# Performance work log

Hardware: AMD Instinct MI355X
Metric: run time of the kernel (lower is better)

Reference implementation:

```python
import jax, jax.numpy as jnp
import numpy as np


def _igd(x, pf):
    # pf: [M, d] reference front, x: [N, d] candidate set
    # squared Euclidean distances via ||a||^2 + ||b||^2 - 2 a.b (cdist expansion)
    pf_sq = jnp.sum(pf * pf, axis=1, keepdims=True)          # [M, 1]
    x_sq = jnp.sum(x * x, axis=1, keepdims=True).T            # [1, N]
    cross = pf @ x.T                                          # [M, N]
    d2 = jnp.maximum(pf_sq + x_sq - 2.0 * cross, 0.0)
    dist = jnp.sqrt(d2)                                       # [M, N]
    # IGD: mean over reference points of min distance to candidate set
    return jnp.mean(jnp.min(dist, axis=1))


def setup_inputs() -> dict:
    key = jax.random.key(0)
    k1, k2 = jax.random.split(key)
    N, M, D = 16384, 16384, 64
    x = jax.random.normal(k1, (N, D), dtype=jnp.float32)
    pf = jax.random.normal(k2, (M, D), dtype=jnp.float32)
    return {"x": x, "pf": pf}


def reference(x, pf):
    return _igd(x, pf)
```

## Files before the change

kernel.cpp:

```cpp
#include <hip/hip_runtime.h>


typedef float f32x16 __attribute__((ext_vector_type(16)));
typedef float f32x2 __attribute__((ext_vector_type(2)));
typedef int i32x8 __attribute__((ext_vector_type(8)));
typedef unsigned long long u64;

#define DIM 64
#define NSPLIT 12
#define UNITB 2048
#define MTILE 256

union BFrag { u64 q[4]; i32x8 v; };

__device__ __forceinline__ void encode16(const float* f, u64 w[2], float& sumsq) {
    unsigned int w32[4];
#pragma unroll
    for (int k = 0; k < 4; ++k) {
        int lo = __builtin_amdgcn_cvt_pk_fp8_f32(f[4 * k],     f[4 * k + 1], 0,  false);
        w32[k] = __builtin_amdgcn_cvt_pk_fp8_f32(f[4 * k + 2], f[4 * k + 3], lo, true);
    }
#pragma unroll
    for (int k = 0; k < 4; ++k) {
        f32x2 d0 = __builtin_amdgcn_cvt_pk_f32_fp8(w32[k], false);
        f32x2 d1 = __builtin_amdgcn_cvt_pk_f32_fp8(w32[k], true);
        sumsq += d0.x * d0.x + d0.y * d0.y + d1.x * d1.x + d1.y * d1.y;
    }
    w[0] = (u64)w32[0] | ((u64)w32[1] << 32);
    w[1] = (u64)w32[2] | ((u64)w32[3] << 32);
}

__global__ void pack_kernel(const float* __restrict__ x, const float* __restrict__ pf,
                            unsigned char* __restrict__ Bp, unsigned char* __restrict__ Ab,
                            float* __restrict__ xsq, float* __restrict__ pfsq,
                            float* __restrict__ out, int N, int M) {
    int gid = blockIdx.x * blockDim.x + threadIdx.x;
    if (gid == 0) out[0] = 0.f;
    if (gid < N * 4) {
        int col = gid >> 2, t = gid & 3;
        const float* s = x + (size_t)col * DIM + t * 16;
        float4 v0 = *(const float4*)(s);
        float4 v1 = *(const float4*)(s + 4);
        float4 v2 = *(const float4*)(s + 8);
        float4 v3 = *(const float4*)(s + 12);
        float f[16] = {v0.x, v0.y, v0.z, v0.w, v1.x, v1.y, v1.z, v1.w,
                       v2.x, v2.y, v2.z, v2.w, v3.x, v3.y, v3.z, v3.w};
        float partial = 0.f;
        u64 w[2];
        encode16(f, w, partial);
        int u = col >> 5, c31 = col & 31;
        unsigned char* ub = Bp + (size_t)u * UNITB;
        int h = t >> 1;
#pragma unroll
        for (int ss = 0; ss < 2; ++ss) {
            int q = (t & 1) * 2 + ss;
            *(u64*)(ub + (size_t)q * 512 + (size_t)(h * 32 + c31) * 8) = w[ss];
        }
        partial += __shfl_xor(partial, 1);
        partial += __shfl_xor(partial, 2);
        if (t == 0) xsq[col] = partial;
    } else {
        int g = gid - N * 4;
        int row = g >> 2, q = g & 3;
        if (row >= M) return;
        const float* s = pf + (size_t)row * DIM + q * 16;
        float4 v0 = *(const float4*)(s);
        float4 v1 = *(const float4*)(s + 4);
        float4 v2 = *(const float4*)(s + 8);
        float4 v3 = *(const float4*)(s + 12);
        float f[16] = {v0.x, v0.y, v0.z, v0.w, v1.x, v1.y, v1.z, v1.w,
                       v2.x, v2.y, v2.z, v2.w, v3.x, v3.y, v3.z, v3.w};
#pragma unroll
        for (int j = 0; j < 16; ++j) f[j] *= -2.f;
        float partial = 0.f;
        u64 w[2];
        encode16(f, w, partial);
        *(u64*)(Ab + (size_t)row * DIM + q * 16)     = w[0];
        *(u64*)(Ab + (size_t)row * DIM + q * 16 + 8) = w[1];
        partial += __shfl_xor(partial, 1);
        partial += __shfl_xor(partial, 2);
        if (q == 0) pfsq[row] = partial * 0.25f;
    }
}

__global__ __launch_bounds__(256, 3)
void igd_main(const unsigned char* __restrict__ A, const unsigned char* __restrict__ Bp,
              const float* __restrict__ xsq, float* __restrict__ partial, int N) {
    const int tid = threadIdx.x;
    const int mTile  = blockIdx.x;
    const int nsplit = blockIdx.y;
    const int lane = tid & 63;
    const int wave = tid >> 6;
    const int half = lane >> 5;
    const int l31  = lane & 31;
    const int rowBase = mTile * MTILE + wave * 64;

    const int utotal = N / 32;
    const int ubase  = utotal / NSPLIT;
    const int urem   = utotal % NSPLIT;
    const int ustart = nsplit * ubase + (nsplit < urem ? nsplit : urem);
    const int ucount = ubase + (nsplit < urem ? 1 : 0);

    BFrag a[2];
#pragma unroll
    for (int g = 0; g < 2; ++g) {
        const unsigned char* ap = A + (size_t)(rowBase + 32 * g + l31) * DIM + half * 32;
#pragma unroll
        for (int qq = 0; qq < 4; ++qq)
            a[g].q[qq] = *(const u64*)(ap + qq * 8);
    }

    const unsigned char* bG = Bp + (size_t)ustart * UNITB + lane * 8;
    const float* xG = xsq + ustart * 32 + l31;

#define LOADG(rr, u)                                                           \
    {                                                                          \
        const unsigned char* p = bG + (size_t)(u) * UNITB;                     \
        rr.q[0] = *(const u64*)(p);                                            \
        rr.q[1] = *(const u64*)(p + 512);                                      \
        rr.q[2] = *(const u64*)(p + 1024);                                     \
        rr.q[3] = *(const u64*)(p + 1536);                                     \
    }

    f32x16 zero, m0, m1;
#pragma unroll
    for (int r = 0; r < 16; ++r) { zero[r] = 0.f; m0[r] = 1e30f; m1[r] = 1e30f; }

#define MFMA2(accA, accB, bfrag)                                               \
    {                                                                          \
        accA = __builtin_amdgcn_mfma_scale_f32_32x32x64_f8f6f4(                \
            a[0].v, bfrag.v, zero, 0, 0, 0, 0x7F7F7F7F, 0, 0x7F7F7F7F);        \
        accB = __builtin_amdgcn_mfma_scale_f32_32x32x64_f8f6f4(                \
            a[1].v, bfrag.v, zero, 0, 0, 0, 0x7F7F7F7F, 0, 0x7F7F7F7F);        \
    }

#define MINS(accA, accB, xq0)                                                  \
    {                                                                          \
        _Pragma("unroll")                                                      \
        for (int r = 0; r < 16; ++r) {                                         \
            m0[r] = fminf(m0[r], accA[r] + (xq0));                             \
            m1[r] = fminf(m1[r], accB[r] + (xq0));                             \
        }                                                                      \
    }

    BFrag b[4];
    float xq[4];
#pragma unroll
    for (int i = 0; i < 4; ++i) {
        LOADG(b[i], i);
        xq[i] = xG[(size_t)i * 32];
    }

    const int umain = ucount & ~3;
    for (int u = 0; u < umain; u += 4) {
#pragma unroll
        for (int s = 0; s < 4; ++s) {
            f32x16 acA, acB;
            MFMA2(acA, acB, b[s]);
            const float x0 = xq[s];
            LOADG(b[s], u + 4 + s);
            xq[s] = xG[(size_t)(u + 4 + s) * 32];
            MINS(acA, acB, x0);
        }
    }
#pragma unroll
    for (int s = 0; s < 3; ++s) {
        if (umain + s < ucount) {
            f32x16 acA, acB;
            MFMA2(acA, acB, b[s]);
            MINS(acA, acB, xq[s]);
        }
    }
#undef LOADG
#undef MFMA2
#undef MINS

#pragma unroll
    for (int mask = 1; mask <= 16; mask <<= 1) {
#pragma unroll
        for (int r = 0; r < 16; ++r) {
            m0[r] = fminf(m0[r], __shfl_xor(m0[r], mask));
            m1[r] = fminf(m1[r], __shfl_xor(m1[r], mask));
        }
    }
    if (l31 == 0) {
#pragma unroll
        for (int r = 0; r < 16; ++r) {
            int row0 = rowBase + (r & 3) + 8 * (r >> 2) + 4 * half;
            partial[(size_t)row0 * NSPLIT + nsplit] = m0[r];
            partial[(size_t)(row0 + 32) * NSPLIT + nsplit] = m1[r];
        }
    }
}

__global__ void reduce_kernel(const float* __restrict__ partial, const float* __restrict__ pfsq,
                              float* __restrict__ out, int M, float invM) {
    int row = blockIdx.x * blockDim.x + threadIdx.x;
    float v = 0.f;
    if (row < M) {
        const float* p = partial + (size_t)row * NSPLIT;
        float mn = 3.4e38f;
#pragma unroll
        for (int s = 0; s < NSPLIT; ++s) mn = fminf(mn, p[s]);
        float d2 = mn + pfsq[row];
        v = sqrtf(fmaxf(d2, 0.f)) * invM;
    }
#pragma unroll
    for (int m = 1; m < 64; m <<= 1) v += __shfl_xor(v, m);
    __shared__ float wsum[4];
    int lane = threadIdx.x & 63, w = threadIdx.x >> 6;
    if (lane == 0) wsum[w] = v;
    __syncthreads();
    if (threadIdx.x == 0) atomicAdd(out, wsum[0] + wsum[1] + wsum[2] + wsum[3]);
}

extern "C" void kernel_launch(void* const* d_in, const int* in_sizes, int n_in,
                              void* d_out, int out_size, void* d_ws, size_t ws_size,
                              hipStream_t stream) {
    const float* x  = (const float*)d_in[0];
    const float* pf = (const float*)d_in[1];
    const int N = in_sizes[0] / DIM;
    const int M = in_sizes[1] / DIM;

    char* ws = (char*)d_ws;
    unsigned char* Bp = (unsigned char*)ws;
    unsigned char* Ab = (unsigned char*)(ws + (size_t)N * DIM);
    float* xsq  = (float*)(ws + (size_t)(N + M) * DIM);
    float* pfsq = xsq + N;
    float* part = pfsq + M;

    int packThreads = (N + M) * 4;
    pack_kernel<<<dim3((packThreads + 255) / 256), 256, 0, stream>>>(
        x, pf, Bp, Ab, xsq, pfsq, (float*)d_out, N, M);
    igd_main<<<dim3(M / MTILE, NSPLIT), 256, 0, stream>>>(Ab, Bp, xsq, part, N);
    reduce_kernel<<<dim3((M + 255) / 256), 256, 0, stream>>>(part, pfsq, (float*)d_out, M, 1.f / (float)M);
}
```

Baseline: 87.29 us.

## Fuse final reduction into main kernel via last-block counter and retile

Removes the separate reduce kernel launch: each M-tile keeps an atomic counter, and the last split block to finish does the min, sqrt and sum for that tile. The tile shrinks to 128 rows (one MFMA per B fragment per wave instead of two), NSPLIT drops to 8, the grid becomes 1D and occupancy is raised to 4 blocks. This trades away a kernel launch and better per-wave register use, but each B fragment now feeds half as much compute and the change adds fences and atomics.

After: 195.6 us. 124% more time.

```diff
diff --git a/kernel.cpp b/kernel.cpp
--- a/kernel.cpp
+++ b/kernel.cpp
@@ -7,9 +7,9 @@
 typedef unsigned long long u64;
 
 #define DIM 64
-#define NSPLIT 12
+#define NSPLIT 8
 #define UNITB 2048
-#define MTILE 256
+#define MTILE 128
 
 union BFrag { u64 q[4]; i32x8 v; };
 
@@ -33,9 +33,10 @@
 __global__ void pack_kernel(const float* __restrict__ x, const float* __restrict__ pf,
                             unsigned char* __restrict__ Bp, unsigned char* __restrict__ Ab,
                             float* __restrict__ xsq, float* __restrict__ pfsq,
-                            float* __restrict__ out, int N, int M) {
+                            int* __restrict__ cnt, float* __restrict__ out, int N, int M) {
     int gid = blockIdx.x * blockDim.x + threadIdx.x;
     if (gid == 0) out[0] = 0.f;
+    if (gid < M / MTILE) cnt[gid] = 0;
     if (gid < N * 4) {
         int col = gid >> 2, t = gid & 3;
         const float* s = x + (size_t)col * DIM + t * 16;
@@ -83,17 +84,20 @@
     }
 }
 
-__global__ __launch_bounds__(256, 3)
+__global__ __launch_bounds__(256, 4)
 void igd_main(const unsigned char* __restrict__ A, const unsigned char* __restrict__ Bp,
-              const float* __restrict__ xsq, float* __restrict__ partial, int N) {
+              const float* __restrict__ xsq, const float* __restrict__ pfsq,
+              float* __restrict__ partial, int* __restrict__ cnt,
+              float* __restrict__ out, int N, int M) {
     const int tid = threadIdx.x;
-    const int mTile  = blockIdx.x;
-    const int nsplit = blockIdx.y;
+    const int mTiles = M / MTILE;
+    const int mTile  = blockIdx.x & (mTiles - 1);
+    const int nsplit = blockIdx.x / mTiles;
     const int lane = tid & 63;
     const int wave = tid >> 6;
     const int half = lane >> 5;
     const int l31  = lane & 31;
-    const int rowBase = mTile * MTILE + wave * 64;
+    const int rowBase = mTile * MTILE + wave * 32;
 
     const int utotal = N / 32;
     const int ubase  = utotal / NSPLIT;
@@ -101,13 +105,12 @@
     const int ustart = nsplit * ubase + (nsplit < urem ? nsplit : urem);
     const int ucount = ubase + (nsplit < urem ? 1 : 0);
 
-    BFrag a[2];
-#pragma unroll
-    for (int g = 0; g < 2; ++g) {
-        const unsigned char* ap = A + (size_t)(rowBase + 32 * g + l31) * DIM + half * 32;
+    BFrag a;
+    {
+        const unsigned char* ap = A + (size_t)(rowBase + l31) * DIM + half * 32;
 #pragma unroll
         for (int qq = 0; qq < 4; ++qq)
-            a[g].q[qq] = *(const u64*)(ap + qq * 8);
+            a.q[qq] = *(const u64*)(ap + qq * 8);
     }
 
     const unsigned char* bG = Bp + (size_t)ustart * UNITB + lane * 8;
@@ -122,25 +125,19 @@
         rr.q[3] = *(const u64*)(p + 1536);                                     \
     }
 
-    f32x16 zero, m0, m1;
-#pragma unroll
-    for (int r = 0; r < 16; ++r) { zero[r] = 0.f; m0[r] = 1e30f; m1[r] = 1e30f; }
-
-#define MFMA2(accA, accB, bfrag)                                               \
-    {                                                                          \
-        accA = __builtin_amdgcn_mfma_scale_f32_32x32x64_f8f6f4(                \
-            a[0].v, bfrag.v, zero, 0, 0, 0, 0x7F7F7F7F, 0, 0x7F7F7F7F);        \
-        accB = __builtin_amdgcn_mfma_scale_f32_32x32x64_f8f6f4(                \
-            a[1].v, bfrag.v, zero, 0, 0, 0, 0x7F7F7F7F, 0, 0x7F7F7F7F);        \
-    }
-
-#define MINS(accA, accB, xq0)                                                  \
+    f32x16 zero, m0;
+#pragma unroll
+    for (int r = 0; r < 16; ++r) { zero[r] = 0.f; m0[r] = 1e30f; }
+
+#define MFMA1(acc, bfrag)                                                      \
+    acc = __builtin_amdgcn_mfma_scale_f32_32x32x64_f8f6f4(                     \
+        a.v, bfrag.v, zero, 0, 0, 0, 0x7F7F7F7F, 0, 0x7F7F7F7F);
+
+#define MINS(acc, xq0)                                                         \
     {                                                                          \
         _Pragma("unroll")                                                      \
-        for (int r = 0; r < 16; ++r) {                                         \
-            m0[r] = fminf(m0[r], accA[r] + (xq0));                             \
-            m1[r] = fminf(m1[r], accB[r] + (xq0));                             \
-        }                                                                      \
+        for (int r = 0; r < 16; ++r)                                           \
+            m0[r] = fminf(m0[r], acc[r] + (xq0));                              \
     }
 
     BFrag b[4];
@@ -155,63 +152,65 @@
     for (int u = 0; u < umain; u += 4) {
 #pragma unroll
         for (int s = 0; s < 4; ++s) {
-            f32x16 acA, acB;
-            MFMA2(acA, acB, b[s]);
+            f32x16 ac;
+            MFMA1(ac, b[s]);
             const float x0 = xq[s];
             LOADG(b[s], u + 4 + s);
             xq[s] = xG[(size_t)(u + 4 + s) * 32];
-            MINS(acA, acB, x0);
+            MINS(ac, x0);
         }
     }
 #pragma unroll
     for (int s = 0; s < 3; ++s) {
         if (umain + s < ucount) {
-            f32x16 acA, acB;
-            MFMA2(acA, acB, b[s]);
-            MINS(acA, acB, xq[s]);
+            f32x16 ac;
+            MFMA1(ac, b[s]);
+            MINS(ac, xq[s]);
         }
     }
 #undef LOADG
-#undef MFMA2
+#undef MFMA1
 #undef MINS
 
 #pragma unroll
     for (int mask = 1; mask <= 16; mask <<= 1) {
 #pragma unroll
-        for (int r = 0; r < 16; ++r) {
+        for (int r = 0; r < 16; ++r)
             m0[r] = fminf(m0[r], __shfl_xor(m0[r], mask));
-            m1[r] = fminf(m1[r], __shfl_xor(m1[r], mask));
-        }
     }
     if (l31 == 0) {
 #pragma unroll
         for (int r = 0; r < 16; ++r) {
             int row0 = rowBase + (r & 3) + 8 * (r >> 2) + 4 * half;
             partial[(size_t)row0 * NSPLIT + nsplit] = m0[r];
-            partial[(size_t)(row0 + 32) * NSPLIT + nsplit] = m1[r];
-        }
-    }
-}
-
-__global__ void reduce_kernel(const float* __restrict__ partial, const float* __restrict__ pfsq,
-                              float* __restrict__ out, int M, float invM) {
-    int row = blockIdx.x * blockDim.x + threadIdx.x;
+        }
+    }
+
+    __shared__ int lastFlag;
+    __syncthreads();
+    __threadfence();
+    if (tid == 0)
+        lastFlag = (atomicAdd(&cnt[mTile], 1) == NSPLIT - 1);
+    __syncthreads();
+    if (!lastFlag) return;
+    __threadfence();
+
     float v = 0.f;
-    if (row < M) {
+    if (tid < MTILE) {
+        int row = mTile * MTILE + tid;
         const float* p = partial + (size_t)row * NSPLIT;
         float mn = 3.4e38f;
 #pragma unroll
         for (int s = 0; s < NSPLIT; ++s) mn = fminf(mn, p[s]);
         float d2 = mn + pfsq[row];
-        v = sqrtf(fmaxf(d2, 0.f)) * invM;
+        v = sqrtf(fmaxf(d2, 0.f)) * (1.f / (float)M);
     }
 #pragma unroll
     for (int m = 1; m < 64; m <<= 1) v += __shfl_xor(v, m);
     __shared__ float wsum[4];
-    int lane = threadIdx.x & 63, w = threadIdx.x >> 6;
-    if (lane == 0) wsum[w] = v;
+    if (lane == 0) wsum[wave] = v;
     __syncthreads();
-    if (threadIdx.x == 0) atomicAdd(out, wsum[0] + wsum[1] + wsum[2] + wsum[3]);
+    if (tid == 0) atomicAdd(out, wsum[0] + wsum[1] + wsum[2] + wsum[3]);
 }
 
 extern "C" void kernel_launch(void* const* d_in, const int* in_sizes, int n_in,
@@ -228,10 +227,11 @@
     float* xsq  = (float*)(ws + (size_t)(N + M) * DIM);
     float* pfsq = xsq + N;
     float* part = pfsq + M;
+    int*   cnt  = (int*)(part + (size_t)M * NSPLIT);
 
     int packThreads = (N + M) * 4;
     pack_kernel<<<dim3((packThreads + 255) / 256), 256, 0, stream>>>(
-        x, pf, Bp, Ab, xsq, pfsq, (float*)d_out, N, M);
-    igd_main<<<dim3(M / MTILE, NSPLIT), 256, 0, stream>>>(Ab, Bp, xsq, part, N);
-    reduce_kernel<<<dim3((M + 255) / 256), 256, 0, stream>>>(part, pfsq, (float*)d_out, M, 1.f / (float)M);
-}
+        x, pf, Bp, Ab, xsq, pfsq, cnt, (float*)d_out, N, M);
+    igd_main<<<dim3((M / MTILE) * NSPLIT), 256, 0, stream>>>(
+        Ab, Bp, xsq, pfsq, part, cnt, (float*)d_out, N, M);
+}
```

## Fuse final reduction into main kernel and fold xsq into MFMA accumulator

Applied to the files above, without the earlier changes.

The separate reduce kernel is removed. The last split block for each M tile, found with an atomic counter, now does the cross-split min, sqrt and mean accumulation. The per-column x norm is also passed as the MFMA C operand, so it is no longer added separately in the min loop. This saves one kernel launch and 32 VALU adds per step, at the cost of an atomic, fences and a tail reduction inside the main kernel.

After: 159.0 us. 82.1% more time.

```diff
diff --git a/kernel.cpp b/kernel.cpp
--- a/kernel.cpp
+++ b/kernel.cpp
@@ -33,9 +33,10 @@
 __global__ void pack_kernel(const float* __restrict__ x, const float* __restrict__ pf,
                             unsigned char* __restrict__ Bp, unsigned char* __restrict__ Ab,
                             float* __restrict__ xsq, float* __restrict__ pfsq,
-                            float* __restrict__ out, int N, int M) {
+                            int* __restrict__ cnt, float* __restrict__ out, int N, int M) {
     int gid = blockIdx.x * blockDim.x + threadIdx.x;
     if (gid == 0) out[0] = 0.f;
+    if (gid < M / MTILE) cnt[gid] = 0;
     if (gid < N * 4) {
         int col = gid >> 2, t = gid & 3;
         const float* s = x + (size_t)col * DIM + t * 16;
@@ -85,7 +86,9 @@
 
 __global__ __launch_bounds__(256, 3)
 void igd_main(const unsigned char* __restrict__ A, const unsigned char* __restrict__ Bp,
-              const float* __restrict__ xsq, float* __restrict__ partial, int N) {
+              const float* __restrict__ xsq, const float* __restrict__ pfsq,
+              float* __restrict__ partial, int* __restrict__ cnt,
+              float* __restrict__ out, int N, int M) {
     const int tid = threadIdx.x;
     const int mTile  = blockIdx.x;
     const int nsplit = blockIdx.y;
@@ -122,24 +125,24 @@
         rr.q[3] = *(const u64*)(p + 1536);                                     \
     }
 
-    f32x16 zero, m0, m1;
-#pragma unroll
-    for (int r = 0; r < 16; ++r) { zero[r] = 0.f; m0[r] = 1e30f; m1[r] = 1e30f; }
-
-#define MFMA2(accA, accB, bfrag)                                               \
+    f32x16 m0, m1;
+#pragma unroll
+    for (int r = 0; r < 16; ++r) { m0[r] = 1e30f; m1[r] = 1e30f; }
+
+#define MFMA2(accA, accB, bfrag, cv)                                           \
     {                                                                          \
         accA = __builtin_amdgcn_mfma_scale_f32_32x32x64_f8f6f4(                \
-            a[0].v, bfrag.v, zero, 0, 0, 0, 0x7F7F7F7F, 0, 0x7F7F7F7F);        \
+            a[0].v, bfrag.v, cv, 0, 0, 0, 0x7F7F7F7F, 0, 0x7F7F7F7F);          \
         accB = __builtin_amdgcn_mfma_scale_f32_32x32x64_f8f6f4(                \
-            a[1].v, bfrag.v, zero, 0, 0, 0, 0x7F7F7F7F, 0, 0x7F7F7F7F);        \
-    }
-
-#define MINS(accA, accB, xq0)                                                  \
+            a[1].v, bfrag.v, cv, 0, 0, 0, 0x7F7F7F7F, 0, 0x7F7F7F7F);          \
+    }
+
+#define MINS(accA, accB)                                                       \
     {                                                                          \
         _Pragma("unroll")                                                      \
         for (int r = 0; r < 16; ++r) {                                         \
-            m0[r] = fminf(m0[r], accA[r] + (xq0));                             \
-            m1[r] = fminf(m1[r], accB[r] + (xq0));                             \
+            m0[r] = fminf(m0[r], accA[r]);                                     \
+            m1[r] = fminf(m1[r], accB[r]);                                     \
         }                                                                      \
     }
 
@@ -155,20 +158,25 @@
     for (int u = 0; u < umain; u += 4) {
 #pragma unroll
         for (int s = 0; s < 4; ++s) {
+            f32x16 cv;
+#pragma unroll
+            for (int r = 0; r < 16; ++r) cv[r] = xq[s];
             f32x16 acA, acB;
-            MFMA2(acA, acB, b[s]);
-            const float x0 = xq[s];
+            MFMA2(acA, acB, b[s], cv);
             LOADG(b[s], u + 4 + s);
             xq[s] = xG[(size_t)(u + 4 + s) * 32];
-            MINS(acA, acB, x0);
+            MINS(acA, acB);
         }
     }
 #pragma unroll
     for (int s = 0; s < 3; ++s) {
         if (umain + s < ucount) {
+            f32x16 cv;
+#pragma unroll
+            for (int r = 0; r < 16; ++r) cv[r] = xq[s];
             f32x16 acA, acB;
-            MFMA2(acA, acB, b[s]);
-            MINS(acA, acB, xq[s]);
+            MFMA2(acA, acB, b[s], cv);
+            MINS(acA, acB);
         }
     }
 #undef LOADG
@@ -191,27 +199,32 @@
             partial[(size_t)(row0 + 32) * NSPLIT + nsplit] = m1[r];
         }
     }
-}
-
-__global__ void reduce_kernel(const float* __restrict__ partial, const float* __restrict__ pfsq,
-                              float* __restrict__ out, int M, float invM) {
-    int row = blockIdx.x * blockDim.x + threadIdx.x;
+
+    __shared__ int lastFlag;
+    __syncthreads();
+    __threadfence();
+    if (tid == 0)
+        lastFlag = (atomicAdd(&cnt[mTile], 1) == NSPLIT - 1);
+    __syncthreads();
+    if (!lastFlag) return;
+    __threadfence();
+
     float v = 0.f;
-    if (row < M) {
+    {
+        int row = mTile * MTILE + tid;
         const float* p = partial + (size_t)row * NSPLIT;
         float mn = 3.4e38f;
 #pragma unroll
         for (int s = 0; s < NSPLIT; ++s) mn = fminf(mn, p[s]);
         float d2 = mn + pfsq[row];
-        v = sqrtf(fmaxf(d2, 0.f)) * invM;
+        v = sqrtf(fmaxf(d2, 0.f)) * (1.f / (float)M);
     }
 #pragma unroll
     for (int m = 1; m < 64; m <<= 1) v += __shfl_xor(v, m);
     __shared__ float wsum[4];
-    int lane = threadIdx.x & 63, w = threadIdx.x >> 6;
-    if (lane == 0) wsum[w] = v;
+    if (lane == 0) wsum[wave] = v;
     __syncthreads();
-    if (threadIdx.x == 0) atomicAdd(out, wsum[0] + wsum[1] + wsum[2] + wsum[3]);
+    if (tid == 0) atomicAdd(out, wsum[0] + wsum[1] + wsum[2] + wsum[3]);
 }
 
 extern "C" void kernel_launch(void* const* d_in, const int* in_sizes, int n_in,
@@ -228,10 +241,11 @@
     float* xsq  = (float*)(ws + (size_t)(N + M) * DIM);
     float* pfsq = xsq + N;
     float* part = pfsq + M;
+    int*   cnt  = (int*)(part + (size_t)M * NSPLIT);
 
     int packThreads = (N + M) * 4;
     pack_kernel<<<dim3((packThreads + 255) / 256), 256, 0, stream>>>(
-        x, pf, Bp, Ab, xsq, pfsq, (float*)d_out, N, M);
-    igd_main<<<dim3(M / MTILE, NSPLIT), 256, 0, stream>>>(Ab, Bp, xsq, part, N);
-    reduce_kernel<<<dim3((M + 255) / 256), 256, 0, stream>>>(part, pfsq, (float*)d_out, M, 1.f / (float)M);
-}
+        x, pf, Bp, Ab, xsq, pfsq, cnt, (float*)d_out, N, M);
+    igd_main<<<dim3(M / MTILE, NSPLIT), 256, 0, stream>>>(
+        Ab, Bp, xsq, pfsq, part, cnt, (float*)d_out, N, M);
+}
```
